# Kernel tuning notes

Measured on AMD Instinct MI355X. Metric: run time of the kernel, lower is better.

## Reference

```python
import jax, jax.numpy as jnp
import numpy as np

K = 16  # number of nearest neighbors (excluding self)
N = 16384


def setup_inputs() -> dict:
    key = jax.random.key(0)
    nodes = jax.random.normal(key, (N, 3), dtype=jnp.float32)
    return {"nodes": nodes}


def reference(nodes):
    n = nodes.shape[0]
    # Pairwise Euclidean distances via the Gram trick:
    # d(i,j)^2 = |x_i|^2 + |x_j|^2 - 2 <x_i, x_j>
    sq = jnp.sum(nodes * nodes, axis=1)                      # [n]
    d2 = sq[:, None] + sq[None, :] - 2.0 * (nodes @ nodes.T)  # [n, n]
    dist = jnp.sqrt(jnp.maximum(d2, 0.0))                    # clamp fp noise
    # k+1 smallest per row (self is nearest with distance ~0), then drop self.
    _, idx = jax.lax.top_k(-dist, K + 1)                     # ascending distance
    idx = idx[:, 1:]                                         # [n, K]
    rows = jnp.arange(n)[:, None]                            # [n, 1]
    adjacency = jnp.zeros((n, n), dtype=jnp.float32).at[rows, idx].set(1.0)
    return adjacency
```

## Files before the change

### kernel.cpp

```cpp
#include <hip/hip_runtime.h>
#include <math.h>

#define NN 16384
#define KK 16
#define RPW 4
#define SW 4
#define RPB (SW * RPW)
#define CAP 512
#define NB 1024
#define NT 64
#define SCAN_BLOCKS (NN / RPB)
#define HALF_F4 (NN * (NN / 4) / 2)

typedef float f32x4 __attribute__((ext_vector_type(4)));
typedef unsigned long long u64;
typedef unsigned short u16;

#define WS_PTS   0
#define WS_PERM  (NN * 16)
#define WS_HIST  (WS_PERM + NN * 4)
#define WS_CUR   (WS_HIST + NB * 4)
#define WS_TMM   (WS_CUR + NB * 4)
#define WS_NB    (WS_TMM + NT * 8)
#define WS_NEED  (WS_NB + (size_t)NN * KK * 2)

__device__ __forceinline__ int xbucket(float x) {
    int b = (int)((x + 6.0f) * (NB / 12.0f));
    return b < 0 ? 0 : (b > NB - 1 ? NB - 1 : b);
}

__global__ __launch_bounds__(1024) void k1_sortfill(const float* __restrict__ nodes,
                                                    float4* __restrict__ pts,
                                                    int* __restrict__ perm,
                                                    int* __restrict__ cur_g,
                                                    float2* __restrict__ tmm_g,
                                                    float* __restrict__ out) {
#pragma clang fp contract(off)
    if (blockIdx.x != 0) {
        const int fidx = blockIdx.x - 1;
        const int tid = fidx * 1024 + threadIdx.x;
        const int nthreads = 512 * 1024;
        f32x4* ob = (f32x4*)out;
        const f32x4 z4 = {0.f, 0.f, 0.f, 0.f};
#pragma unroll 4
        for (int k = 0; k < HALF_F4 / nthreads; ++k)
            __builtin_nontemporal_store(z4, ob + (size_t)k * nthreads + tid);
        return;
    }
    __shared__ int sh[NB];
    __shared__ int shc[NB];
    const int t = threadIdx.x;
    sh[t] = 0;
    __syncthreads();
    for (int i = t; i < NN; i += 1024)
        atomicAdd(&sh[xbucket(nodes[3 * i])], 1);
    __syncthreads();
    const int h0 = sh[t];
    for (int o = 1; o < NB; o <<= 1) {
        const int v = (t >= o) ? sh[t - o] : 0;
        __syncthreads();
        sh[t] += v;
        __syncthreads();
    }
    shc[t] = sh[t] - h0;
    __syncthreads();
    for (int i = t; i < NN; i += 1024) {
        const float x = nodes[3 * i], y = nodes[3 * i + 1], z = nodes[3 * i + 2];
        const float sq = (x * x + y * y) + z * z;
        const int pos = atomicAdd(&shc[xbucket(x)], 1);
        pts[pos] = make_float4(x, y, z, sq);
        perm[pos] = i;
    }
    __syncthreads();
    cur_g[t] = shc[t];
    const int lane = t & 63, w = t >> 6;
    for (int tt = w; tt < NT; tt += 16) {
        float mn = INFINITY, mx = -INFINITY;
#pragma unroll
        for (int e = 0; e < 4; ++e) {
            const float x = pts[tt * 256 + e * 64 + lane].x;
            mn = fminf(mn, x); mx = fmaxf(mx, x);
        }
#pragma unroll
        for (int s = 1; s <= 32; s <<= 1) {
            mn = fminf(mn, __shfl_xor(mn, s));
            mx = fmaxf(mx, __shfl_xor(mx, s));
        }
        if (lane == 0) tmm_g[tt] = make_float2(mn, mx);
    }
}

__device__ __forceinline__ float bcastf(float v, int l) {
    return __int_as_float(__builtin_amdgcn_readlane(__float_as_int(v), l));
}
__device__ __forceinline__ bool lexless(float da, int ia, float db, int ib) {
    return (da < db) || ((da == db) && (ia < ib));
}
__device__ __forceinline__ void insert_tile(bool rough, float d2, int j,
                                            float& ld, int& li,
                                            float& td, int& ti, float& td2u,
                                            int lane) {
#pragma clang fp contract(off)
    if (!__any(rough)) return;
    float dist = INFINITY;
    if (rough) dist = sqrtf(fmaxf(d2, 0.0f));
    bool done = false;
    while (true) {
        const bool pass = (!done) && rough && lexless(dist, j, td, ti);
        const u64 m = __ballot(pass);
        if (m == 0ull) break;
        const int src = __ffsll(m) - 1;
        const float dc = __shfl(dist, src);
        const int   ic = __shfl(j, src);
        if (lane == src) done = true;
        const bool gt = lexless(dc, ic, ld, li);
        const u64 gm = __ballot(gt);
        const int p = __ffsll(gm) - 1;
        const float pd = __shfl_up(ld, 1);
        const int   pi = __shfl_up(li, 1);
        if (gt) {
            if (lane == p) { ld = dc; li = ic; }
            else           { ld = pd; li = pi; }
        }
        td = __shfl(ld, 16);
        ti = __shfl(li, 16);
        td2u = td * td * 1.000001f;
    }
}

__device__ __forceinline__ void scan_body(int sblock,
                                          const float4* __restrict__ pts,
                                          const int* __restrict__ perm,
                                          const int* __restrict__ cur,
                                          const float2* __restrict__ tmm_g,
                                          const float* __restrict__ nodes,
                                          float* __restrict__ out,
                                          u16* __restrict__ nbws) {
#pragma clang fp contract(off)
    const int lane = threadIdx.x & 63;
    const int wid  = threadIdx.x >> 6;
    const int tid  = threadIdx.x;
    const int rowBase = sblock * RPB;

    __shared__ float2 tmm[NT];
    __shared__ u16 buf[SW][RPW][CAP];
    __shared__ u64 sel[SW][CAP];
    __shared__ int cnt[SW][RPW];

    if (tid < NT) tmm[tid] = tmm_g[tid];
    __syncthreads();

    float xs[RPW], ys[RPW], zs[RPW], ss[RPW];
    int tc[RPW];
#pragma unroll
    for (int r = 0; r < RPW; ++r) {
        const int row = rowBase + wid * RPW + r;
        xs[r] = nodes[3 * row];
        ys[r] = nodes[3 * row + 1];
        zs[r] = nodes[3 * row + 2];
        ss[r] = (xs[r] * xs[r] + ys[r] * ys[r]) + zs[r] * zs[r];
        int t = (cur[xbucket(xs[r])] - 1) >> 8;
        t = t - 1; t = t < 0 ? 0 : (t > NT - 3 ? NT - 3 : t);
        tc[r] = t;
    }

    float rm[RPW];
#pragma unroll
    for (int r = 0; r < RPW; ++r) rm[r] = INFINITY;
#pragma unroll
    for (int r = 0; r < RPW; ++r) {
        for (int tt = 0; tt < 3; ++tt) {
            const int tb = (tc[r] + tt) * 256;
            const float4 q0 = pts[tb + lane];
            const float4 q1 = pts[tb + 64 + lane];
            const float4 q2 = pts[tb + 128 + lane];
            const float4 q3 = pts[tb + 192 + lane];
            const float d0 = (ss[r] + q0.w) - 2.0f * fmaf(zs[r], q0.z, fmaf(ys[r], q0.y, xs[r] * q0.x));
            const float d1 = (ss[r] + q1.w) - 2.0f * fmaf(zs[r], q1.z, fmaf(ys[r], q1.y, xs[r] * q1.x));
            const float d2 = (ss[r] + q2.w) - 2.0f * fmaf(zs[r], q2.z, fmaf(ys[r], q2.y, xs[r] * q2.x));
            const float d3 = (ss[r] + q3.w) - 2.0f * fmaf(zs[r], q3.z, fmaf(ys[r], q3.y, xs[r] * q3.x));
            rm[r] = fminf(rm[r], fminf(fminf(d0, d1), fminf(d2, d3)));
        }
    }
    float sv[RPW];
#pragma unroll
    for (int r = 0; r < RPW; ++r) sv[r] = rm[r];
#pragma unroll
    for (int k = 2; k <= 64; k <<= 1) {
#pragma unroll
        for (int j = k >> 1; j >= 1; j >>= 1) {
            const bool keepmin = (((lane & j) == 0) == ((lane & k) == 0));
#pragma unroll
            for (int r = 0; r < RPW; ++r) {
                const float o = __shfl_xor(sv[r], j);
                sv[r] = keepmin ? fminf(sv[r], o) : fmaxf(sv[r], o);
            }
        }
    }
    float tau[RPW];
#pragma unroll
    for (int r = 0; r < RPW; ++r)
        tau[r] = fmaxf(bcastf(sv[r], 16), 0.0f) * 1.000002f + 1e-30f;

    if (lane < RPW) cnt[wid][lane] = 0;
    asm volatile("s_waitcnt lgkmcnt(0)" ::: "memory");

    for (int t = 0; t < NT; ++t) {
        const float2 mm = tmm[t];
        bool kp[RPW]; bool anyk = false;
#pragma unroll
        for (int r = 0; r < RPW; ++r) {
            const float dx = fmaxf(fmaxf(mm.x - xs[r], xs[r] - mm.y), 0.0f);
            kp[r] = (dx * dx <= tau[r] * 1.00001f + 5e-5f);
            anyk |= kp[r];
        }
        if (!anyk) continue;
        const int base = t * 256;
        const float4 q0 = pts[base + lane];
        const float4 q1 = pts[base + 64 + lane];
        const float4 q2 = pts[base + 128 + lane];
        const float4 q3 = pts[base + 192 + lane];
#pragma unroll
        for (int r = 0; r < RPW; ++r) {
            if (!kp[r]) continue;
            const float d0 = (ss[r] + q0.w) - 2.0f * fmaf(zs[r], q0.z, fmaf(ys[r], q0.y, xs[r] * q0.x));
            const float d1 = (ss[r] + q1.w) - 2.0f * fmaf(zs[r], q1.z, fmaf(ys[r], q1.y, xs[r] * q1.x));
            const float d2 = (ss[r] + q2.w) - 2.0f * fmaf(zs[r], q2.z, fmaf(ys[r], q2.y, xs[r] * q2.x));
            const float d3 = (ss[r] + q3.w) - 2.0f * fmaf(zs[r], q3.z, fmaf(ys[r], q3.y, xs[r] * q3.x));
            const bool p0 = d0 <= tau[r], p1 = d1 <= tau[r];
            const bool p2 = d2 <= tau[r], p3 = d3 <= tau[r];
            if (p0 | p1 | p2 | p3) {
                if (p0) { const int o = atomicAdd(&cnt[wid][r], 1);
                          if (o < CAP) buf[wid][r][o] = (u16)(base + lane); }
                if (p1) { const int o = atomicAdd(&cnt[wid][r], 1);
                          if (o < CAP) buf[wid][r][o] = (u16)(base + 64 + lane); }
                if (p2) { const int o = atomicAdd(&cnt[wid][r], 1);
                          if (o < CAP) buf[wid][r][o] = (u16)(base + 128 + lane); }
                if (p3) { const int o = atomicAdd(&cnt[wid][r], 1);
                          if (o < CAP) buf[wid][r][o] = (u16)(base + 192 + lane); }
            }
        }
    }
    asm volatile("s_waitcnt lgkmcnt(0)" ::: "memory");

#pragma unroll
    for (int r = 0; r < RPW; ++r) {
        const int C = cnt[wid][r];
        const int row = rowBase + wid * RPW + r;
        if (C <= CAP) {
            for (int e = lane; e < C; e += 64) {
                const int si = (int)buf[wid][r][e];
                const float4 q = pts[si];
                const float dd = (ss[r] + q.w) - 2.0f * fmaf(zs[r], q.z, fmaf(ys[r], q.y, xs[r] * q.x));
                const float dist = sqrtf(fmaxf(dd, 0.0f));
                sel[wid][e] = (((u64)__float_as_uint(dist)) << 32) | (unsigned)perm[si];
            }
            asm volatile("s_waitcnt lgkmcnt(0) vmcnt(0)" ::: "memory");
            for (int e = lane; e < C; e += 64) {
                const u64 my = sel[wid][e];
                int rk = 0;
                for (int c = 0; c < C; ++c)
                    rk += (sel[wid][c] < my) ? 1 : 0;
                if (rk >= 1 && rk <= KK) {
                    if (nbws) nbws[(size_t)row * KK + rk - 1] = (u16)(my & 0xffffu);
                    else      out[(size_t)row * NN + (int)(my & 0xffffffffu)] = 1.0f;
                }
            }
            asm volatile("s_waitcnt lgkmcnt(0)" ::: "memory");
        } else {
            float ld = INFINITY; int li = 0x7fffffff;
            float td = INFINITY; int ti = 0x7fffffff; float t2 = INFINITY;
            for (int tt = 0; tt < NN / 64; ++tt) {
                const int j = tt * 64 + lane;
                const float4 q = pts[j];
                const int oi = perm[j];
                const float dd = (ss[r] + q.w) - 2.0f * fmaf(zs[r], q.z, fmaf(ys[r], q.y, xs[r] * q.x));
                insert_tile(dd <= t2, dd, oi, ld, li, td, ti, t2, lane);
            }
            if (lane >= 1 && lane <= KK) {
                if (nbws) nbws[(size_t)row * KK + lane - 1] = (u16)li;
                else      out[(size_t)row * NN + li] = 1.0f;
            }
        }
    }
}

__global__ __launch_bounds__(256) void k2_mega(const float4* __restrict__ pts,
                                               const int* __restrict__ perm,
                                               const int* __restrict__ cur,
                                               const float2* __restrict__ tmm_g,
                                               const float* __restrict__ nodes,
                                               float* __restrict__ out,
                                               u16* __restrict__ nbws) {
    const int b = blockIdx.x;
    if (b & 1) {
        const int fidx = b >> 1;
        const int tid = fidx * 256 + threadIdx.x;
        const int nthreads = 1024 * 256;
        f32x4* ob = (f32x4*)out + (size_t)HALF_F4;
        const f32x4 z4 = {0.f, 0.f, 0.f, 0.f};
#pragma unroll 4
        for (int k = 0; k < HALF_F4 / nthreads; ++k)
            __builtin_nontemporal_store(z4, ob + (size_t)k * nthreads + tid);
    } else {
        scan_body(b >> 1, pts, perm, cur, tmm_g, nodes, nullptr, nbws);
    }
}

__global__ __launch_bounds__(256) void ones_kernel(const u16* __restrict__ nbws,
                                                   float* __restrict__ out) {
    const int t = blockIdx.x * 256 + threadIdx.x;
    const int row = t >> 4;
    out[(size_t)row * NN + nbws[t]] = 1.0f;
}

__global__ __launch_bounds__(256) void fill_zero_full(f32x4* __restrict__ ob) {
    const int tid = blockIdx.x * 256 + threadIdx.x;
    const int nthreads = 2048 * 256;
    const f32x4 z4 = {0.f, 0.f, 0.f, 0.f};
#pragma unroll 4
    for (int k = 0; k < (NN * (NN / 4)) / nthreads; ++k)
        __builtin_nontemporal_store(z4, ob + (size_t)k * nthreads + tid);
}

__global__ __launch_bounds__(256) void knn_scan_direct(const float4* __restrict__ pts,
                                                       const int* __restrict__ perm,
                                                       const int* __restrict__ cur,
                                                       const float2* __restrict__ tmm_g,
                                                       const float* __restrict__ nodes,
                                                       float* __restrict__ out) {
    scan_body(blockIdx.x, pts, perm, cur, tmm_g, nodes, out, nullptr);
}

extern "C" void kernel_launch(void* const* d_in, const int* in_sizes, int n_in,
                              void* d_out, int out_size, void* d_ws, size_t ws_size,
                              hipStream_t stream) {
    const float* nodes = (const float*)d_in[0];
    float* out = (float*)d_out;
    (void)in_sizes; (void)n_in; (void)out_size;

    char* ws = (char*)d_ws;
    float4* pts  = (float4*)(ws + WS_PTS);
    int*    perm = (int*)   (ws + WS_PERM);
    int*    cur  = (int*)   (ws + WS_CUR);
    float2* tmm  = (float2*)(ws + WS_TMM);
    u16*    nbws = (u16*)   (ws + WS_NB);

    if (ws_size >= WS_NEED) {
        hipLaunchKernelGGL(k1_sortfill, dim3(513), dim3(1024), 0, stream,
                           nodes, pts, perm, cur, tmm, out);
        hipLaunchKernelGGL(k2_mega, dim3(2 * SCAN_BLOCKS), dim3(256), 0, stream,
                           pts, perm, cur, tmm, nodes, out, nbws);
        hipLaunchKernelGGL(ones_kernel, dim3(NN * KK / 256), dim3(256), 0, stream,
                           nbws, out);
    } else {
        hipLaunchKernelGGL(k1_sortfill, dim3(1), dim3(1024), 0, stream,
                           nodes, pts, perm, cur, tmm, out);
        hipLaunchKernelGGL(fill_zero_full, dim3(2048), dim3(256), 0, stream,
                           (f32x4*)out);
        hipLaunchKernelGGL(knn_scan_direct, dim3(SCAN_BLOCKS), dim3(256), 0, stream,
                           pts, perm, cur, tmm, nodes, out);
    }
}
```

Before: 325.1 us.

## Move all zero-fill from sort kernel into mega kernel filler blocks

```diff
diff --git a/kernel.cpp b/kernel.cpp
--- a/kernel.cpp
+++ b/kernel.cpp
@@ -10,7 +10,7 @@
 #define NB 1024
 #define NT 64
 #define SCAN_BLOCKS (NN / RPB)
-#define HALF_F4 (NN * (NN / 4) / 2)
+#define MEGA_FILL 1024
 
 typedef float f32x4 __attribute__((ext_vector_type(4)));
 typedef unsigned long long u64;
@@ -29,24 +29,12 @@
     return b < 0 ? 0 : (b > NB - 1 ? NB - 1 : b);
 }
 
-__global__ __launch_bounds__(1024) void k1_sortfill(const float* __restrict__ nodes,
-                                                    float4* __restrict__ pts,
-                                                    int* __restrict__ perm,
-                                                    int* __restrict__ cur_g,
-                                                    float2* __restrict__ tmm_g,
-                                                    float* __restrict__ out) {
+__global__ __launch_bounds__(1024) void k_sort(const float* __restrict__ nodes,
+                                               float4* __restrict__ pts,
+                                               int* __restrict__ perm,
+                                               int* __restrict__ cur_g,
+                                               float2* __restrict__ tmm_g) {
 #pragma clang fp contract(off)
-    if (blockIdx.x != 0) {
-        const int fidx = blockIdx.x - 1;
-        const int tid = fidx * 1024 + threadIdx.x;
-        const int nthreads = 512 * 1024;
-        f32x4* ob = (f32x4*)out;
-        const f32x4 z4 = {0.f, 0.f, 0.f, 0.f};
-#pragma unroll 4
-        for (int k = 0; k < HALF_F4 / nthreads; ++k)
-            __builtin_nontemporal_store(z4, ob + (size_t)k * nthreads + tid);
-        return;
-    }
     __shared__ int sh[NB];
     __shared__ int shc[NB];
     const int t = threadIdx.x;
@@ -285,22 +273,22 @@
     }
 }
 
-__global__ __launch_bounds__(256) void k2_mega(const float4* __restrict__ pts,
-                                               const int* __restrict__ perm,
-                                               const int* __restrict__ cur,
-                                               const float2* __restrict__ tmm_g,
-                                               const float* __restrict__ nodes,
-                                               float* __restrict__ out,
-                                               u16* __restrict__ nbws) {
+__global__ __launch_bounds__(256) void k_mega(const float4* __restrict__ pts,
+                                              const int* __restrict__ perm,
+                                              const int* __restrict__ cur,
+                                              const float2* __restrict__ tmm_g,
+                                              const float* __restrict__ nodes,
+                                              float* __restrict__ out,
+                                              u16* __restrict__ nbws) {
     const int b = blockIdx.x;
     if (b & 1) {
         const int fidx = b >> 1;
         const int tid = fidx * 256 + threadIdx.x;
-        const int nthreads = 1024 * 256;
-        f32x4* ob = (f32x4*)out + (size_t)HALF_F4;
+        const int nthreads = MEGA_FILL * 256;
+        f32x4* ob = (f32x4*)out;
         const f32x4 z4 = {0.f, 0.f, 0.f, 0.f};
 #pragma unroll 4
-        for (int k = 0; k < HALF_F4 / nthreads; ++k)
+        for (int k = 0; k < (NN * (NN / 4)) / nthreads; ++k)
             __builtin_nontemporal_store(z4, ob + (size_t)k * nthreads + tid);
     } else {
         scan_body(b >> 1, pts, perm, cur, tmm_g, nodes, nullptr, nbws);
@@ -346,16 +334,15 @@
     float2* tmm  = (float2*)(ws + WS_TMM);
     u16*    nbws = (u16*)   (ws + WS_NB);
 
+    hipLaunchKernelGGL(k_sort, dim3(1), dim3(1024), 0, stream,
+                       nodes, pts, perm, cur, tmm);
+
     if (ws_size >= WS_NEED) {
-        hipLaunchKernelGGL(k1_sortfill, dim3(513), dim3(1024), 0, stream,
-                           nodes, pts, perm, cur, tmm, out);
-        hipLaunchKernelGGL(k2_mega, dim3(2 * SCAN_BLOCKS), dim3(256), 0, stream,
+        hipLaunchKernelGGL(k_mega, dim3(2 * SCAN_BLOCKS), dim3(256), 0, stream,
                            pts, perm, cur, tmm, nodes, out, nbws);
         hipLaunchKernelGGL(ones_kernel, dim3(NN * KK / 256), dim3(256), 0, stream,
                            nbws, out);
     } else {
-        hipLaunchKernelGGL(k1_sortfill, dim3(1), dim3(1024), 0, stream,
-                           nodes, pts, perm, cur, tmm, out);
         hipLaunchKernelGGL(fill_zero_full, dim3(2048), dim3(256), 0, stream,
                            (f32x4*)out);
         hipLaunchKernelGGL(knn_scan_direct, dim3(SCAN_BLOCKS), dim3(256), 0, stream,
```

Result: faster. 261.9 us (median of 2 runs) (-19.4%).
